# Kernel optimization log

Measured on AMD Instinct MI355X. Metric: run time of the kernel, lower is better.

Reference implementation:

```python
import jax, jax.numpy as jnp
import numpy as np

D_MODEL = 1024
NUM_HEADS = 16
HEAD_DIM = D_MODEL // NUM_HEADS
B, S = 4, 2048


def _xavier(key, shape, gain=0.1):
    fan_in, fan_out = shape[1], shape[0]
    a = gain * np.sqrt(6.0 / (fan_in + fan_out))
    return jax.random.uniform(key, shape, jnp.float32, -a, a)


def setup_inputs() -> dict:
    key = jax.random.key(0)
    ks = jax.random.split(key, 11)
    inp = {
        "q": jax.random.normal(ks[0], (B, S, D_MODEL), jnp.float32),
        "k": jax.random.normal(ks[1], (B, S, D_MODEL), jnp.float32),
        "v": jax.random.normal(ks[2], (B, S, D_MODEL), jnp.float32),
        # nn.Linear weights are [out, in]; y = x @ W.T + b
        "Wq": _xavier(ks[3], (D_MODEL, D_MODEL)),
        "bq": jnp.zeros((D_MODEL,), jnp.float32),
        "Wk": _xavier(ks[4], (D_MODEL, D_MODEL)),
        "bk": jnp.zeros((D_MODEL,), jnp.float32),
        "Wv": _xavier(ks[5], (D_MODEL, D_MODEL)),
        "bv": jnp.zeros((D_MODEL,), jnp.float32),
        "Wo": _xavier(ks[6], (D_MODEL, D_MODEL)),
        "bo": jnp.zeros((D_MODEL,), jnp.float32),
    }
    return inp


def reference(q, k, v, Wq, bq, Wk, bk, Wv, bv, Wo, bo):
    b = q.shape[0]
    qh = (q @ Wq.T + bq).reshape(b, -1, NUM_HEADS, HEAD_DIM).transpose(0, 2, 1, 3)
    kh = (k @ Wk.T + bk).reshape(b, -1, NUM_HEADS, HEAD_DIM).transpose(0, 2, 1, 3)
    vh = (v @ Wv.T + bv).reshape(b, -1, NUM_HEADS, HEAD_DIM).transpose(0, 2, 1, 3)
    # NOTE: original (buggy) module scales by sqrt(d_model), not sqrt(head_dim)
    scale = 1.0 / jnp.sqrt(jnp.float32(D_MODEL))
    scores = jnp.einsum('bhqd,bhkd->bhqk', qh, kh) * scale  # [B,H,S,S]
    attn = jax.nn.softmax(scores, axis=-1)
    out = jnp.einsum('bhqk,bhkd->bhqd', attn, vh)
    out = out.transpose(0, 2, 1, 3).reshape(b, -1, D_MODEL)
    return out @ Wo.T + bo
```

## Files before the change

### kernel.cpp

```cpp
#include <hip/hip_runtime.h>

typedef unsigned short u16;
typedef short bf16x8 __attribute__((ext_vector_type(8)));
typedef float f32x4 __attribute__((ext_vector_type(4)));
typedef u16 u16x8 __attribute__((ext_vector_type(8)));

__device__ __forceinline__ u16 f2bf(float f) {
  unsigned u = __float_as_uint(f);
  u = u + 0x7fffu + ((u >> 16) & 1u);
  return (u16)(u >> 16);
}

#define GLD16(ldsp, gp)                                                         \
  __builtin_amdgcn_global_load_lds(                                             \
      (__attribute__((address_space(1))) void*)(void*)(gp),                     \
      (__attribute__((address_space(3))) void*)(ldsp), 16, 0, 0)

#define CVTPK(dst, lo, hi)                                                      \
  asm("v_cvt_pk_bf16_f32 %0, %1, %2" : "=v"(dst) : "v"(lo), "v"(hi))
#define PACK8(dst, a0, a1, a2, a3, a4, a5, a6, a7)                              \
  do {                                                                          \
    union { unsigned u_[4]; bf16x8 v_; } c_;                                    \
    CVTPK(c_.u_[0], a0, a1); CVTPK(c_.u_[1], a2, a3);                           \
    CVTPK(c_.u_[2], a4, a5); CVTPK(c_.u_[3], a6, a7);                           \
    dst = c_.v_;                                                                \
  } while (0)

__global__ __launch_bounds__(256) void pack_bf16(const float* __restrict__ in,
                                                 u16* __restrict__ out, int n8) {
  int i = blockIdx.x * blockDim.x + threadIdx.x;
  if (i >= n8) return;
  const float4* p = (const float4*)in + (size_t)i * 2;
  float4 a = p[0], b = p[1];
  u16x8 r;
  r[0] = f2bf(a.x); r[1] = f2bf(a.y); r[2] = f2bf(a.z); r[3] = f2bf(a.w);
  r[4] = f2bf(b.x); r[5] = f2bf(b.y); r[6] = f2bf(b.z); r[7] = f2bf(b.w);
  *(u16x8*)(out + (size_t)i * 8) = r;
}

__global__ __launch_bounds__(256) void pack_w4(const float* __restrict__ w0,
                                               const float* __restrict__ w1,
                                               const float* __restrict__ w2,
                                               const float* __restrict__ w3,
                                               u16* __restrict__ out) {
  int i = blockIdx.x * 256 + threadIdx.x;
  int which = i >> 17;
  const float* src = which == 0 ? w0 : which == 1 ? w1 : which == 2 ? w2 : w3;
  int j = i & 131071;
  const float4* p = (const float4*)src + (size_t)j * 2;
  float4 a = p[0], b = p[1];
  u16x8 r;
  r[0] = f2bf(a.x); r[1] = f2bf(a.y); r[2] = f2bf(a.z); r[3] = f2bf(a.w);
  r[4] = f2bf(b.x); r[5] = f2bf(b.y); r[6] = f2bf(b.z); r[7] = f2bf(b.w);
  *(u16x8*)(out + (size_t)i * 8) = r;
}

template <int EPI>
__global__ __launch_bounds__(256, 2)
void gemm_bt(const u16* __restrict__ A, const u16* __restrict__ B,
             const float* __restrict__ bias, void* __restrict__ outp) {
  constexpr int K = 1024;
  __shared__ __align__(16) u16 As[128 * 64];
  __shared__ __align__(16) u16 Bs[128 * 64];
  const int t = threadIdx.x;
  const int w = t >> 6;
  const int l = t & 63;
  const int lr = l & 15, lg = l >> 4;
  const int flat = blockIdx.x | (blockIdx.y << 3);
  const int swz = ((flat & 7) << 6) | (flat >> 3);
  const int row0 = (swz >> 3) * 128, col0 = (swz & 7) * 128;
  const int wm = (w >> 1) * 64, wn = (w & 1) * 64;

  f32x4 acc[4][4] = {};

  const int srow = t >> 3;
  const int scol = ((t & 7) ^ (srow & 7)) * 8;
  const u16* gA = A + (size_t)(row0 + srow) * K + scol;
  const u16* gB = B + (size_t)(col0 + srow) * K + scol;
  u16* lA = &As[w * 512];
  u16* lB = &Bs[w * 512];

  for (int k0 = 0; k0 < K; k0 += 64) {
#pragma unroll
    for (int j = 0; j < 4; ++j) {
      GLD16(lA + j * 2048, gA + (size_t)j * 32 * K + k0);
      GLD16(lB + j * 2048, gB + (size_t)j * 32 * K + k0);
    }
    __syncthreads();
#pragma unroll
    for (int kh2 = 0; kh2 < 2; ++kh2) {
      bf16x8 aF[4], bF[4];
      const int bc = (kh2 * 64 + lg * 16) ^ ((lr & 7) * 16);
#pragma unroll
      for (int mi = 0; mi < 4; ++mi)
        aF[mi] = *(const bf16x8*)((const char*)As + (wm + mi * 16 + lr) * 128 + bc);
#pragma unroll
      for (int ni = 0; ni < 4; ++ni)
        bF[ni] = *(const bf16x8*)((const char*)Bs + (wn + ni * 16 + lr) * 128 + bc);
#pragma unroll
      for (int mi = 0; mi < 4; ++mi)
#pragma unroll
        for (int ni = 0; ni < 4; ++ni)
          acc[mi][ni] = __builtin_amdgcn_mfma_f32_16x16x32_bf16(aF[mi], bF[ni],
                                                                acc[mi][ni], 0, 0, 0);
    }
    __syncthreads();
  }

#pragma unroll
  for (int mi = 0; mi < 4; ++mi) {
#pragma unroll
    for (int ni = 0; ni < 4; ++ni) {
      const int n = col0 + wn + ni * 16 + lr;
      const float bv = bias[n];
#pragma unroll
      for (int r = 0; r < 4; ++r) {
        const int m = row0 + wm + mi * 16 + lg * 4 + r;
        const float v = acc[mi][ni][r] + bv;
        if (EPI == 0) {
          int b = m >> 11, s = m & 2047, h = n >> 6, d = n & 63;
          ((u16*)outp)[((size_t)((b << 4) + h) * 2048 + s) * 64 + d] = f2bf(v);
        } else if (EPI == 1) {
          int b = m >> 11, s = m & 2047, h = n >> 6, d = n & 63;
          int bh = (b << 4) + h, tile = s >> 6, kp = s & 63;
          int kM = kp >> 5, k5 = kp & 31;
          int kpp = kM * 32 + ((k5 >> 2) & 3) * 8 + (k5 >> 4) * 4 + (k5 & 3);
          int chunk = (kpp >> 3) ^ (d & 7);
          ((u16*)outp)[((size_t)bh << 17) + tile * 4096 + d * 64 + chunk * 8 + (kpp & 7)]
              = f2bf(v);
        } else {
          ((float*)outp)[(size_t)m * 1024 + n] = v;
        }
      }
    }
  }
}

__global__ __launch_bounds__(256, 3)
void attn_fwd(const u16* __restrict__ qh, const u16* __restrict__ kh,
              const u16* __restrict__ vp, u16* __restrict__ aout) {
  __shared__ __align__(16) u16 Ks[2][4096];
  __shared__ __align__(16) u16 Vl[2][4096];
  const int t = threadIdx.x;
  const int w = t >> 6, l = t & 63;
  const int lr = l & 15, lg = l >> 4;
  const int flat = blockIdx.x | (blockIdx.y << 4);
  const int swz = ((flat & 7) << 7) | (flat >> 3);
  const int qb = swz & 15, bh = swz >> 4;
  const int q0 = qb * 128 + w * 32;

  bf16x8 qf[2][2];
#pragma unroll
  for (int qi = 0; qi < 2; ++qi) {
    const u16* qp = qh + ((size_t)bh * 2048 + q0 + qi * 16 + lr) * 64 + lg * 8;
    qf[qi][0] = *(const bf16x8*)qp;
    qf[qi][1] = *(const bf16x8*)(qp + 32);
  }

  f32x4 o0[4] = {}, o1[4] = {};
  float lsum0 = 0.f, lsum1 = 0.f;

  const int krow = t >> 3, kseg = t & 7;
  const u16* gK = kh + ((size_t)bh * 2048 + krow) * 64 + ((kseg ^ (krow & 7)) * 8);
  const u16* gV = vp + ((size_t)bh << 17) + t * 8;

  const int xo0 = (lg * 16) ^ ((lr & 7) * 16);
  const int xo1 = (64 + lg * 16) ^ ((lr & 7) * 16);

  {
    u16* kd = &Ks[0][0] + w * 512;
    u16* vd = &Vl[0][0] + w * 512;
    GLD16(kd, gK); GLD16(kd + 2048, gK + 2048);
    GLD16(vd, gV); GLD16(vd + 2048, gV + 2048);
    gK += 4096; gV += 4096;
  }
  __syncthreads();

  for (int tix = 0; tix < 32; ++tix) {
    const int cur = tix & 1;
    if (tix < 31) {
      u16* kd = &Ks[cur ^ 1][0] + w * 512;
      u16* vd = &Vl[cur ^ 1][0] + w * 512;
      GLD16(kd, gK); GLD16(kd + 2048, gK + 2048);
      GLD16(vd, gV); GLD16(vd + 2048, gV + 2048);
      gK += 4096; gV += 4096;
    }
    const char* kb = (const char*)&Ks[cur][0];
    f32x4 s0[4], s1[4];
#pragma unroll
    for (int cq = 0; cq < 4; ++cq) {
      const char* rowp = kb + (cq * 16 + lr) * 128;
      bf16x8 kf0 = *(const bf16x8*)(rowp + xo0);
      bf16x8 kf1 = *(const bf16x8*)(rowp + xo1);
      f32x4 a = {}, b2 = {};
      a  = __builtin_amdgcn_mfma_f32_16x16x32_bf16(kf0, qf[0][0], a, 0, 0, 0);
      a  = __builtin_amdgcn_mfma_f32_16x16x32_bf16(kf1, qf[0][1], a, 0, 0, 0);
      b2 = __builtin_amdgcn_mfma_f32_16x16x32_bf16(kf0, qf[1][0], b2, 0, 0, 0);
      b2 = __builtin_amdgcn_mfma_f32_16x16x32_bf16(kf1, qf[1][1], b2, 0, 0, 0);
      s0[cq] = a; s1[cq] = b2;
    }
    float p0[16], p1[16];
#pragma unroll
    for (int cq = 0; cq < 4; ++cq)
#pragma unroll
      for (int r = 0; r < 4; ++r) {
        p0[cq * 4 + r] = __expf(s0[cq][r] * 0.03125f);
        p1[cq * 4 + r] = __expf(s1[cq][r] * 0.03125f);
      }
    float a0 = 0.f, a1 = 0.f;
#pragma unroll
    for (int i = 0; i < 16; ++i) { a0 += p0[i]; a1 += p1[i]; }
    lsum0 += a0; lsum1 += a1;
    bf16x8 pA0, pA1, pB0, pB1;
    PACK8(pA0, p0[0], p0[1], p0[2], p0[3], p0[4], p0[5], p0[6], p0[7]);
    PACK8(pA1, p0[8], p0[9], p0[10], p0[11], p0[12], p0[13], p0[14], p0[15]);
    PACK8(pB0, p1[0], p1[1], p1[2], p1[3], p1[4], p1[5], p1[6], p1[7]);
    PACK8(pB1, p1[8], p1[9], p1[10], p1[11], p1[12], p1[13], p1[14], p1[15]);
    const char* vbb = (const char*)&Vl[cur][0];
#pragma unroll
    for (int dc = 0; dc < 4; ++dc) {
      const char* rp = vbb + (dc * 16 + lr) * 128;
      bf16x8 vA = *(const bf16x8*)(rp + xo0);
      bf16x8 vB = *(const bf16x8*)(rp + xo1);
      o0[dc] = __builtin_amdgcn_mfma_f32_16x16x32_bf16(pA0, vA, o0[dc], 0, 0, 0);
      o0[dc] = __builtin_amdgcn_mfma_f32_16x16x32_bf16(pA1, vB, o0[dc], 0, 0, 0);
      o1[dc] = __builtin_amdgcn_mfma_f32_16x16x32_bf16(pB0, vA, o1[dc], 0, 0, 0);
      o1[dc] = __builtin_amdgcn_mfma_f32_16x16x32_bf16(pB1, vB, o1[dc], 0, 0, 0);
    }
    __syncthreads();
  }

  float sA = lsum0; sA += __shfl_xor(sA, 16); sA += __shfl_xor(sA, 32);
  float sB = lsum1; sB += __shfl_xor(sB, 16); sB += __shfl_xor(sB, 32);
  const int b = bh >> 4, h = bh & 15;
#pragma unroll
  for (int r = 0; r < 4; ++r) {
    const float dA = 1.f / __shfl(sA, lg * 4 + r);
    const float dB = 1.f / __shfl(sB, lg * 4 + r);
    const size_t rowA = (size_t)b * 2048 + q0 + lg * 4 + r;
#pragma unroll
    for (int dc = 0; dc < 4; ++dc) {
      aout[rowA * 1024 + h * 64 + dc * 16 + lr] = f2bf(o0[dc][r] * dA);
      aout[(rowA + 16) * 1024 + h * 64 + dc * 16 + lr] = f2bf(o1[dc][r] * dB);
    }
  }
}

extern "C" void kernel_launch(void* const* d_in, const int* in_sizes, int n_in,
                              void* d_out, int out_size, void* d_ws, size_t ws_size,
                              hipStream_t stream) {
  const float* q  = (const float*)d_in[0];
  const float* k  = (const float*)d_in[1];
  const float* v  = (const float*)d_in[2];
  const float* Wq = (const float*)d_in[3];
  const float* bq = (const float*)d_in[4];
  const float* Wk = (const float*)d_in[5];
  const float* bk = (const float*)d_in[6];
  const float* Wv = (const float*)d_in[7];
  const float* bv = (const float*)d_in[8];
  const float* Wo = (const float*)d_in[9];
  const float* bo = (const float*)d_in[10];

  char* ws = (char*)d_ws;
  u16* wbf = (u16*)(ws);
  u16* xbf = (u16*)(ws + (8ull << 20));
  u16* qhB = (u16*)(ws + (24ull << 20));
  u16* khB = (u16*)(ws + (40ull << 20));
  u16* vtB = (u16*)(ws + (56ull << 20));
  u16* aout = xbf;

  pack_w4<<<2048, 256, 0, stream>>>(Wq, Wk, Wv, Wo, wbf);

  const int XN8 = 8192 * 1024 / 8;
  dim3 gg(8, 64), gb(256);
  pack_bf16<<<4096, 256, 0, stream>>>(q, xbf, XN8);
  gemm_bt<0><<<gg, gb, 0, stream>>>(xbf, wbf + (0u << 20), bq, qhB);
  pack_bf16<<<4096, 256, 0, stream>>>(k, xbf, XN8);
  gemm_bt<0><<<gg, gb, 0, stream>>>(xbf, wbf + (1u << 20), bk, khB);
  pack_bf16<<<4096, 256, 0, stream>>>(v, xbf, XN8);
  gemm_bt<1><<<gg, gb, 0, stream>>>(xbf, wbf + (2u << 20), bv, vtB);
  attn_fwd<<<dim3(16, 64), 256, 0, stream>>>(qhB, khB, vtB, aout);
  gemm_bt<2><<<gg, gb, 0, stream>>>(aout, wbf + (3u << 20), bo, d_out);

  (void)in_sizes; (void)n_in; (void)out_size; (void)ws_size;
}
```

Measured before the change: 208.1 us.

## Fuse fp32-to-bf16 input conversion into a batched QKV GEMM and tune softmax

Removes the three separate pack_bf16 passes: the new gemm_qkv kernel loads fp32 activations directly, converts them in registers and writes them to LDS. Q, K and V projections run in one launch with a z grid dimension. The softmax scale is folded into Q together with log2(e) so attention can use a raw exp2. The row sums are computed with MFMA against a vector of ones instead of VALU adds and shuffles, and s_setprio hints are placed around the MFMA sections. The A-tile load becomes a register-staged fp32 path rather than async LDS loads, which may add register pressure and expose latency.

Measured after the change: 172.1 us. 1.21x faster.

```diff
diff --git a/kernel.cpp b/kernel.cpp
--- a/kernel.cpp
+++ b/kernel.cpp
@@ -9,6 +9,14 @@
   unsigned u = __float_as_uint(f);
   u = u + 0x7fffu + ((u >> 16) & 1u);
   return (u16)(u >> 16);
+}
+
+__device__ __forceinline__ float fexp2(float x) {
+#if __has_builtin(__builtin_amdgcn_exp2f)
+  return __builtin_amdgcn_exp2f(x);
+#else
+  return exp2f(x);
+#endif
 }
 
 #define GLD16(ldsp, gp)                                                         \
@@ -25,18 +33,6 @@
     CVTPK(c_.u_[2], a4, a5); CVTPK(c_.u_[3], a6, a7);                           \
     dst = c_.v_;                                                                \
   } while (0)
-
-__global__ __launch_bounds__(256) void pack_bf16(const float* __restrict__ in,
-                                                 u16* __restrict__ out, int n8) {
-  int i = blockIdx.x * blockDim.x + threadIdx.x;
-  if (i >= n8) return;
-  const float4* p = (const float4*)in + (size_t)i * 2;
-  float4 a = p[0], b = p[1];
-  u16x8 r;
-  r[0] = f2bf(a.x); r[1] = f2bf(a.y); r[2] = f2bf(a.z); r[3] = f2bf(a.w);
-  r[4] = f2bf(b.x); r[5] = f2bf(b.y); r[6] = f2bf(b.z); r[7] = f2bf(b.w);
-  *(u16x8*)(out + (size_t)i * 8) = r;
-}
 
 __global__ __launch_bounds__(256) void pack_w4(const float* __restrict__ w0,
                                                const float* __restrict__ w1,
@@ -55,10 +51,113 @@
   *(u16x8*)(out + (size_t)i * 8) = r;
 }
 
-template <int EPI>
 __global__ __launch_bounds__(256, 2)
-void gemm_bt(const u16* __restrict__ A, const u16* __restrict__ B,
-             const float* __restrict__ bias, void* __restrict__ outp) {
+void gemm_qkv(const float* __restrict__ qi, const float* __restrict__ ki,
+              const float* __restrict__ vi, const u16* __restrict__ wbf,
+              const float* __restrict__ bq, const float* __restrict__ bk,
+              const float* __restrict__ bv, u16* __restrict__ qo,
+              u16* __restrict__ ko, u16* __restrict__ vo) {
+  constexpr int K = 1024;
+  __shared__ __align__(16) u16 As[128 * 64];
+  __shared__ __align__(16) u16 Bs[128 * 64];
+  const int z = blockIdx.z;
+  const float* Af = z == 0 ? qi : z == 1 ? ki : vi;
+  const u16* Bw = wbf + ((size_t)z << 20);
+  const float* bias = z == 0 ? bq : z == 1 ? bk : bv;
+
+  const int t = threadIdx.x;
+  const int w = t >> 6, l = t & 63;
+  const int lr = l & 15, lg = l >> 4;
+  const int flat = blockIdx.x | (blockIdx.y << 3);
+  const int swz = ((flat & 7) << 6) | (flat >> 3);
+  const int row0 = (swz >> 3) * 128, col0 = (swz & 7) * 128;
+  const int wm = (w >> 1) * 64, wn = (w & 1) * 64;
+
+  f32x4 acc[4][4] = {};
+
+  const int ar = t >> 3;
+  const int xw = ((t & 7) ^ (ar & 7)) * 16;
+  const float* gA = Af + (size_t)(row0 + ar) * K + (t & 7) * 8;
+  const u16* gB = Bw + (size_t)(col0 + ar) * K + (((t & 7) ^ (ar & 7)) * 8);
+  u16* lB = &Bs[w * 512];
+
+  float4 a0[4], a1[4];
+#pragma unroll
+  for (int j = 0; j < 4; ++j) {
+    const float* p = gA + (size_t)j * 32 * K;
+    a0[j] = *(const float4*)p;
+    a1[j] = *(const float4*)(p + 4);
+  }
+
+  for (int kt = 0; kt < 16; ++kt) {
+#pragma unroll
+    for (int j = 0; j < 4; ++j) {
+      bf16x8 c;
+      PACK8(c, a0[j].x, a0[j].y, a0[j].z, a0[j].w, a1[j].x, a1[j].y, a1[j].z, a1[j].w);
+      *(bf16x8*)((char*)As + (ar + j * 32) * 128 + xw) = c;
+    }
+#pragma unroll
+    for (int j = 0; j < 4; ++j)
+      GLD16(lB + j * 2048, gB + (size_t)j * 32 * K + kt * 64);
+    if (kt < 15) {
+#pragma unroll
+      for (int j = 0; j < 4; ++j) {
+        const float* p = gA + (size_t)j * 32 * K + (kt + 1) * 64;
+        a0[j] = *(const float4*)p;
+        a1[j] = *(const float4*)(p + 4);
+      }
+    }
+    __syncthreads();
+#pragma unroll
+    for (int kh2 = 0; kh2 < 2; ++kh2) {
+      bf16x8 aF[4], bF[4];
+      const int bc = (kh2 * 64 + lg * 16) ^ ((lr & 7) * 16);
+#pragma unroll
+      for (int mi = 0; mi < 4; ++mi)
+        aF[mi] = *(const bf16x8*)((const char*)As + (wm + mi * 16 + lr) * 128 + bc);
+#pragma unroll
+      for (int ni = 0; ni < 4; ++ni)
+        bF[ni] = *(const bf16x8*)((const char*)Bs + (wn + ni * 16 + lr) * 128 + bc);
+#pragma unroll
+      for (int mi = 0; mi < 4; ++mi)
+#pragma unroll
+        for (int ni = 0; ni < 4; ++ni)
+          acc[mi][ni] = __builtin_amdgcn_mfma_f32_16x16x32_bf16(aF[mi], bF[ni],
+                                                                acc[mi][ni], 0, 0, 0);
+    }
+    __syncthreads();
+  }
+
+#pragma unroll
+  for (int mi = 0; mi < 4; ++mi) {
+#pragma unroll
+    for (int ni = 0; ni < 4; ++ni) {
+      const int n = col0 + wn + ni * 16 + lr;
+      const float bvv = bias[n];
+#pragma unroll
+      for (int r = 0; r < 4; ++r) {
+        const int m = row0 + wm + mi * 16 + lg * 4 + r;
+        const float vv = acc[mi][ni][r] + bvv;
+        const int bI = m >> 11, s = m & 2047, h = n >> 6, d = n & 63;
+        if (z == 0) {
+          qo[((size_t)((bI << 4) + h) * 2048 + s) * 64 + d] = f2bf(vv * 0.045084223f);
+        } else if (z == 1) {
+          ko[((size_t)((bI << 4) + h) * 2048 + s) * 64 + d] = f2bf(vv);
+        } else {
+          int bh = (bI << 4) + h, tile = s >> 6, kp = s & 63;
+          int kM = kp >> 5, k5 = kp & 31;
+          int kpp = kM * 32 + ((k5 >> 2) & 3) * 8 + (k5 >> 4) * 4 + (k5 & 3);
+          int chunk = (kpp >> 3) ^ (d & 7);
+          vo[((size_t)bh << 17) + tile * 4096 + d * 64 + chunk * 8 + (kpp & 7)] = f2bf(vv);
+        }
+      }
+    }
+  }
+}
+
+__global__ __launch_bounds__(256, 2)
+void gemm_out(const u16* __restrict__ A, const u16* __restrict__ B,
+              const float* __restrict__ bias, float* __restrict__ outp) {
   constexpr int K = 1024;
   __shared__ __align__(16) u16 As[128 * 64];
   __shared__ __align__(16) u16 Bs[128 * 64];
@@ -108,7 +207,7 @@
   }
 
 #pragma unroll
-  for (int mi = 0; mi < 4; ++mi) {
+  for (int mi = 0; mi < 4; ++mi)
 #pragma unroll
     for (int ni = 0; ni < 4; ++ni) {
       const int n = col0 + wn + ni * 16 + lr;
@@ -116,24 +215,9 @@
 #pragma unroll
       for (int r = 0; r < 4; ++r) {
         const int m = row0 + wm + mi * 16 + lg * 4 + r;
-        const float v = acc[mi][ni][r] + bv;
-        if (EPI == 0) {
-          int b = m >> 11, s = m & 2047, h = n >> 6, d = n & 63;
-          ((u16*)outp)[((size_t)((b << 4) + h) * 2048 + s) * 64 + d] = f2bf(v);
-        } else if (EPI == 1) {
-          int b = m >> 11, s = m & 2047, h = n >> 6, d = n & 63;
-          int bh = (b << 4) + h, tile = s >> 6, kp = s & 63;
-          int kM = kp >> 5, k5 = kp & 31;
-          int kpp = kM * 32 + ((k5 >> 2) & 3) * 8 + (k5 >> 4) * 4 + (k5 & 3);
-          int chunk = (kpp >> 3) ^ (d & 7);
-          ((u16*)outp)[((size_t)bh << 17) + tile * 4096 + d * 64 + chunk * 8 + (kpp & 7)]
-              = f2bf(v);
-        } else {
-          ((float*)outp)[(size_t)m * 1024 + n] = v;
-        }
+        outp[(size_t)m * 1024 + n] = acc[mi][ni][r] + bv;
       }
     }
-  }
 }
 
 __global__ __launch_bounds__(256, 3)
@@ -158,14 +242,15 @@
   }
 
   f32x4 o0[4] = {}, o1[4] = {};
-  float lsum0 = 0.f, lsum1 = 0.f;
+  f32x4 sm0 = {}, sm1 = {};
+  const bf16x8 ones = {16256, 16256, 16256, 16256, 16256, 16256, 16256, 16256};
 
   const int krow = t >> 3, kseg = t & 7;
   const u16* gK = kh + ((size_t)bh * 2048 + krow) * 64 + ((kseg ^ (krow & 7)) * 8);
   const u16* gV = vp + ((size_t)bh << 17) + t * 8;
 
   const int xo0 = (lg * 16) ^ ((lr & 7) * 16);
-  const int xo1 = (64 + lg * 16) ^ ((lr & 7) * 16);
+  const int xo1 = xo0 ^ 64;
 
   {
     u16* kd = &Ks[0][0] + w * 512;
@@ -187,6 +272,7 @@
     }
     const char* kb = (const char*)&Ks[cur][0];
     f32x4 s0[4], s1[4];
+    __builtin_amdgcn_s_setprio(1);
 #pragma unroll
     for (int cq = 0; cq < 4; ++cq) {
       const char* rowp = kb + (cq * 16 + lr) * 128;
@@ -199,23 +285,25 @@
       b2 = __builtin_amdgcn_mfma_f32_16x16x32_bf16(kf1, qf[1][1], b2, 0, 0, 0);
       s0[cq] = a; s1[cq] = b2;
     }
+    __builtin_amdgcn_s_setprio(0);
     float p0[16], p1[16];
 #pragma unroll
     for (int cq = 0; cq < 4; ++cq)
 #pragma unroll
       for (int r = 0; r < 4; ++r) {
-        p0[cq * 4 + r] = __expf(s0[cq][r] * 0.03125f);
-        p1[cq * 4 + r] = __expf(s1[cq][r] * 0.03125f);
+        p0[cq * 4 + r] = fexp2(s0[cq][r]);
+        p1[cq * 4 + r] = fexp2(s1[cq][r]);
       }
-    float a0 = 0.f, a1 = 0.f;
-#pragma unroll
-    for (int i = 0; i < 16; ++i) { a0 += p0[i]; a1 += p1[i]; }
-    lsum0 += a0; lsum1 += a1;
     bf16x8 pA0, pA1, pB0, pB1;
     PACK8(pA0, p0[0], p0[1], p0[2], p0[3], p0[4], p0[5], p0[6], p0[7]);
     PACK8(pA1, p0[8], p0[9], p0[10], p0[11], p0[12], p0[13], p0[14], p0[15]);
     PACK8(pB0, p1[0], p1[1], p1[2], p1[3], p1[4], p1[5], p1[6], p1[7]);
     PACK8(pB1, p1[8], p1[9], p1[10], p1[11], p1[12], p1[13], p1[14], p1[15]);
+    __builtin_amdgcn_s_setprio(1);
+    sm0 = __builtin_amdgcn_mfma_f32_16x16x32_bf16(pA0, ones, sm0, 0, 0, 0);
+    sm0 = __builtin_amdgcn_mfma_f32_16x16x32_bf16(pA1, ones, sm0, 0, 0, 0);
+    sm1 = __builtin_amdgcn_mfma_f32_16x16x32_bf16(pB0, ones, sm1, 0, 0, 0);
+    sm1 = __builtin_amdgcn_mfma_f32_16x16x32_bf16(pB1, ones, sm1, 0, 0, 0);
     const char* vbb = (const char*)&Vl[cur][0];
 #pragma unroll
     for (int dc = 0; dc < 4; ++dc) {
@@ -227,16 +315,15 @@
       o1[dc] = __builtin_amdgcn_mfma_f32_16x16x32_bf16(pB0, vA, o1[dc], 0, 0, 0);
       o1[dc] = __builtin_amdgcn_mfma_f32_16x16x32_bf16(pB1, vB, o1[dc], 0, 0, 0);
     }
-    __syncthreads();
-  }
-
-  float sA = lsum0; sA += __shfl_xor(sA, 16); sA += __shfl_xor(sA, 32);
-  float sB = lsum1; sB += __shfl_xor(sB, 16); sB += __shfl_xor(sB, 32);
+    __builtin_amdgcn_s_setprio(0);
+    __syncthreads();
+  }
+
   const int b = bh >> 4, h = bh & 15;
 #pragma unroll
   for (int r = 0; r < 4; ++r) {
-    const float dA = 1.f / __shfl(sA, lg * 4 + r);
-    const float dB = 1.f / __shfl(sB, lg * 4 + r);
+    const float dA = 1.f / sm0[r];
+    const float dB = 1.f / sm1[r];
     const size_t rowA = (size_t)b * 2048 + q0 + lg * 4 + r;
 #pragma unroll
     for (int dc = 0; dc < 4; ++dc) {
@@ -262,25 +349,18 @@
   const float* bo = (const float*)d_in[10];
 
   char* ws = (char*)d_ws;
-  u16* wbf = (u16*)(ws);
-  u16* xbf = (u16*)(ws + (8ull << 20));
-  u16* qhB = (u16*)(ws + (24ull << 20));
-  u16* khB = (u16*)(ws + (40ull << 20));
-  u16* vtB = (u16*)(ws + (56ull << 20));
-  u16* aout = xbf;
+  u16* wbf  = (u16*)(ws);
+  u16* aout = (u16*)(ws + (8ull << 20));
+  u16* qhB  = (u16*)(ws + (24ull << 20));
+  u16* khB  = (u16*)(ws + (40ull << 20));
+  u16* vtB  = (u16*)(ws + (56ull << 20));
 
   pack_w4<<<2048, 256, 0, stream>>>(Wq, Wk, Wv, Wo, wbf);
-
-  const int XN8 = 8192 * 1024 / 8;
-  dim3 gg(8, 64), gb(256);
-  pack_bf16<<<4096, 256, 0, stream>>>(q, xbf, XN8);
-  gemm_bt<0><<<gg, gb, 0, stream>>>(xbf, wbf + (0u << 20), bq, qhB);
-  pack_bf16<<<4096, 256, 0, stream>>>(k, xbf, XN8);
-  gemm_bt<0><<<gg, gb, 0, stream>>>(xbf, wbf + (1u << 20), bk, khB);
-  pack_bf16<<<4096, 256, 0, stream>>>(v, xbf, XN8);
-  gemm_bt<1><<<gg, gb, 0, stream>>>(xbf, wbf + (2u << 20), bv, vtB);
+  gemm_qkv<<<dim3(8, 64, 3), 256, 0, stream>>>(q, k, v, wbf, bq, bk, bv,
+                                               qhB, khB, vtB);
   attn_fwd<<<dim3(16, 64), 256, 0, stream>>>(qhB, khB, vtB, aout);
-  gemm_bt<2><<<gg, gb, 0, stream>>>(aout, wbf + (3u << 20), bo, d_out);
+  gemm_out<<<dim3(8, 64), 256, 0, stream>>>(aout, wbf + (3u << 20), bo,
+                                            (float*)d_out);
 
   (void)in_sizes; (void)n_in; (void)out_size; (void)ws_size;
 }
```
